# Kernel optimization log

Measured on AMD Instinct MI355X. Metric: run time of the kernel, lower is better.

## Reference

```python
import jax, jax.numpy as jnp
import numpy as np

N_NODES = 100000
N_EDGES = 3200000
N_GRAPHS = 512
IN_CH = 128
HID = 32
OUT = 2


def setup_inputs() -> dict:
    key = jax.random.key(0)
    ks = jax.random.split(key, 6)
    x = jax.random.normal(ks[0], (N_NODES, IN_CH), dtype=jnp.float32)
    edge_index = jax.random.randint(ks[1], (2, N_EDGES), 0, N_NODES, dtype=jnp.int64)
    batch = jnp.sort(jax.random.randint(ks[2], (N_NODES,), 0, N_GRAPHS, dtype=jnp.int64))
    # Glorot-ish params
    W1 = jax.random.normal(ks[3], (IN_CH, HID), dtype=jnp.float32) * (1.0 / np.sqrt(IN_CH))
    b1 = jnp.zeros((HID,), dtype=jnp.float32)
    W2 = jax.random.normal(ks[4], (HID, HID), dtype=jnp.float32) * (1.0 / np.sqrt(HID))
    b2 = jnp.zeros((HID,), dtype=jnp.float32)
    Wl = jax.random.normal(ks[5], (HID, OUT), dtype=jnp.float32) * (1.0 / np.sqrt(HID))
    bl = jnp.zeros((OUT,), dtype=jnp.float32)
    return {"x": x, "edge_index": edge_index, "batch": batch,
            "W1": W1, "b1": b1, "W2": W2, "b2": b2, "Wl": Wl, "bl": bl}


def _gcn_conv(h, src, dst, W, b, n_nodes):
    # PyG GCNConv: transform, add self-loops, symmetric deg normalization,
    # scatter-add messages from src -> dst, then bias.
    h = h @ W  # [N, F_out]
    ones = jnp.ones(src.shape[0], dtype=h.dtype)
    # degree on target nodes, +1 for the implicit self-loop
    deg = jax.ops.segment_sum(ones, dst, num_segments=n_nodes) + 1.0
    dinv = jax.lax.rsqrt(deg)  # deg >= 1 always
    norm = dinv[src] * dinv[dst]  # [E]
    agg = jax.ops.segment_sum(h[src] * norm[:, None], dst, num_segments=n_nodes)
    # self-loop contribution: norm_ii = dinv_i^2
    agg = agg + h * (dinv * dinv)[:, None]
    return agg + b


def reference(x, edge_index, batch, W1, b1, W2, b2, Wl, bl):
    n_nodes = x.shape[0]
    src, dst = edge_index[0], edge_index[1]
    h = jax.nn.relu(_gcn_conv(x, src, dst, W1, b1, n_nodes))
    h = jax.nn.relu(_gcn_conv(h, src, dst, W2, b2, n_nodes))
    # global mean pool per graph
    sums = jax.ops.segment_sum(h, batch, num_segments=N_GRAPHS)
    counts = jax.ops.segment_sum(jnp.ones(n_nodes, h.dtype), batch, num_segments=N_GRAPHS)
    pooled = sums / jnp.maximum(counts, 1.0)[:, None]  # [G, 32]
    return pooled @ Wl + bl  # [G, 2]
```

## Files before the change

kernel.cpp:

```cpp
#include <hip/hip_runtime.h>
#include <hip/hip_bf16.h>

#define N_NODES 100000
#define N_EDGES 3200000
#define N_GRAPHS 512
#define NBUK 782
#define CAP 4608
#define FILL_CHUNK 8192
#define FILL_BLOCKS ((N_EDGES + FILL_CHUNK - 1) / FILL_CHUNK)
#define GEMM1_BLOCKS ((N_NODES + 63) / 64)

__device__ __forceinline__ float blo(unsigned v) { return __uint_as_float(v << 16); }
__device__ __forceinline__ float bhi(unsigned v) { return __uint_as_float(v & 0xffff0000u); }

__global__ __launch_bounds__(1024) void k_fatA(const int* __restrict__ ei,
                                               int* __restrict__ gcnt,
                                               unsigned* __restrict__ packed,
                                               const float* __restrict__ x,
                                               const float* __restrict__ W1,
                                               float* __restrict__ H1u) {
    __shared__ __align__(16) char smem[49152];
    int t = threadIdx.x;
    if (blockIdx.x < FILL_BLOCKS) {
        unsigned* buf = (unsigned*)smem;
        int* h    = (int*)(smem + 32768);
        int* base = (int*)(smem + 35896);
        int* sb   = (int*)(smem + 39024);
        int* sc   = (int*)(smem + 42152);
        for (int i = t; i < NBUK; i += 1024) h[i] = 0;
        __syncthreads();
        int s0 = blockIdx.x * FILL_CHUNK;
        int ng = min(FILL_CHUNK, N_EDGES - s0) >> 2;
        const int4* src4 = (const int4*)(ei + s0);
        const int4* dst4 = (const int4*)(ei + N_EDGES + s0);
        int4 sv[2], dv[2];
        int  rk[2][4];
#pragma unroll
        for (int g = 0; g < 2; g++) {
            int gi = t + g * 1024;
            if (gi < ng) {
                sv[g] = src4[gi];
                dv[g] = dst4[gi];
                rk[g][0] = atomicAdd(&h[dv[g].x >> 7], 1);
                rk[g][1] = atomicAdd(&h[dv[g].y >> 7], 1);
                rk[g][2] = atomicAdd(&h[dv[g].z >> 7], 1);
                rk[g][3] = atomicAdd(&h[dv[g].w >> 7], 1);
            }
        }
        __syncthreads();
        for (int i = t; i < NBUK; i += 1024) {
            int c = h[i];
            base[i] = c ? atomicAdd(&gcnt[i], c) : 0;
        }
        sc[t] = (t < NBUK) ? h[t] : 0;
        __syncthreads();
        for (int off = 1; off < 1024; off <<= 1) {
            int v = (t >= off) ? sc[t - off] : 0;
            __syncthreads();
            sc[t] += v;
            __syncthreads();
        }
        for (int i = t; i < NBUK; i += 1024) sb[i] = sc[i] - h[i];
        __syncthreads();
#pragma unroll
        for (int g = 0; g < 2; g++) {
            int gi = t + g * 1024;
            if (gi < ng) {
                int s[4] = {sv[g].x, sv[g].y, sv[g].z, sv[g].w};
                int d[4] = {dv[g].x, dv[g].y, dv[g].z, dv[g].w};
#pragma unroll
                for (int k = 0; k < 4; k++) {
                    int bk = d[k] >> 7;
                    buf[sb[bk] + rk[g][k]] = (unsigned)s[k] | (((unsigned)d[k] & 127u) << 17);
                }
            }
        }
        __syncthreads();
        int w = t >> 6, lane = t & 63;
        for (int bk = w; bk < NBUK; bk += 16) {
            int c = h[bk];
            if (!c) continue;
            unsigned* gp = packed + (size_t)bk * CAP + base[bk];
            int lb = sb[bk];
            for (int j = lane; j < c; j += 64) gp[j] = buf[lb + j];
        }
    } else {
        float* Ws = (float*)smem;
        float* xs = (float*)(smem + 16384);
        int b = blockIdx.x - FILL_BLOCKS;
        ((float4*)Ws)[t] = ((const float4*)W1)[t];
        int row0 = b * 64;
        const float4* x4 = (const float4*)(x + (size_t)row0 * 128);
        float4* xs4 = (float4*)xs;
        int maxr = min(64, N_NODES - row0);
        int nf4 = maxr * 32;
#pragma unroll
        for (int i = 0; i < 8; i++) {
            int idx = t + i * 1024;
            if (idx < nf4) xs4[idx] = x4[idx];
        }
        __syncthreads();
        int col = t & 31;
        int g = t >> 5;
        int r0 = 2 * g, r1 = 2 * g + 1;
        const float4* xa4 = xs4 + r0 * 32;
        const float4* xb4 = xs4 + r1 * 32;
        float a0 = 0.f, a1 = 0.f;
#pragma unroll 8
        for (int k4 = 0; k4 < 32; k4++) {
            float4 xa = xa4[k4];
            float4 xb = xb4[k4];
            float w0 = Ws[(k4 * 4 + 0) * 32 + col];
            float w1 = Ws[(k4 * 4 + 1) * 32 + col];
            float w2 = Ws[(k4 * 4 + 2) * 32 + col];
            float w3 = Ws[(k4 * 4 + 3) * 32 + col];
            a0 += xa.x * w0 + xa.y * w1 + xa.z * w2 + xa.w * w3;
            a1 += xb.x * w0 + xb.y * w1 + xb.z * w2 + xb.w * w3;
        }
        if (row0 + r0 < N_NODES) H1u[(size_t)(row0 + r0) * 32 + col] = a0;
        if (row0 + r1 < N_NODES) H1u[(size_t)(row0 + r1) * 32 + col] = a1;
    }
}

__global__ __launch_bounds__(512) void k_csr(const unsigned* __restrict__ packed,
                                             const int* __restrict__ gcnt,
                                             int* __restrict__ rp, int* __restrict__ rpe,
                                             float* __restrict__ dinv,
                                             int* __restrict__ csr,
                                             const float* __restrict__ H1u,
                                             __hip_bfloat16* __restrict__ H1s) {
    __shared__ int deg[128];
    __shared__ int sd[128];
    __shared__ int nb0[128];
    __shared__ float dsh[128];
    __shared__ int lcsr[CAP] __attribute__((aligned(16)));
    int t = threadIdx.x;
    int b = blockIdx.x;
    if (t < 128) deg[t] = 0;
    __syncthreads();
    int n = gcnt[b];
    const unsigned* pb = packed + (size_t)b * CAP;
    unsigned pv[3][4];
    int rk[3][4];
#pragma unroll
    for (int g = 0; g < 3; g++) {
        int i0 = 4 * (t + g * 512);
        if (i0 < n) {
            if (i0 + 3 < n) {
                uint4 p = *(const uint4*)(pb + i0);
                pv[g][0] = p.x; pv[g][1] = p.y; pv[g][2] = p.z; pv[g][3] = p.w;
            } else {
#pragma unroll
                for (int k = 0; k < 4; k++) pv[g][k] = (i0 + k < n) ? pb[i0 + k] : 0u;
            }
#pragma unroll
            for (int k = 0; k < 4; k++)
                if (i0 + k < n) rk[g][k] = atomicAdd(&deg[pv[g][k] >> 17], 1);
        }
    }
    __syncthreads();
    int d = (t < 128) ? deg[t] : 0;
    if (t < 128) sd[t] = d;
    __syncthreads();
    for (int off = 1; off < 128; off <<= 1) {
        int v = (t >= off && t < 128) ? sd[t - off] : 0;
        __syncthreads();
        if (t < 128) sd[t] += v;
        __syncthreads();
    }
    if (t < 128) {
        int l0 = sd[t] - d;
        nb0[t] = l0;
        float di = rsqrtf((float)d + 1.0f);
        dsh[t] = di;
        int node = b * 128 + t;
        if (node < N_NODES) {
            rp[node] = b * CAP + l0;
            rpe[node] = b * CAP + l0 + d;
            dinv[node] = di;
        }
    }
    __syncthreads();
#pragma unroll
    for (int g = 0; g < 3; g++) {
        int i0 = 4 * (t + g * 512);
        if (i0 < n) {
#pragma unroll
            for (int k = 0; k < 4; k++) {
                if (i0 + k < n) {
                    unsigned p = pv[g][k];
                    lcsr[nb0[p >> 17] + rk[g][k]] = (int)(p & 0x1FFFFu);
                }
            }
        }
    }
    __syncthreads();
    int n4 = (n + 3) >> 2;
    int4* dst4 = (int4*)(csr + (size_t)b * CAP);
    const int4* sl4 = (const int4*)lcsr;
    for (int i = t; i < n4; i += 512) dst4[i] = sl4[i];
    for (int i = t; i < 1024; i += 512) {
        int row = i >> 3, q = i & 7;
        int node = b * 128 + row;
        if (node < N_NODES) {
            float4 v = ((const float4*)H1u)[(size_t)node * 8 + q];
            float di = dsh[row];
            __hip_bfloat16 tmp[4];
            tmp[0] = __float2bfloat16(v.x * di);
            tmp[1] = __float2bfloat16(v.y * di);
            tmp[2] = __float2bfloat16(v.z * di);
            tmp[3] = __float2bfloat16(v.w * di);
            *(uint2*)(H1s + (size_t)node * 32 + q * 4) = *(uint2*)tmp;
        }
    }
}

__global__ void k_gather(const __hip_bfloat16* __restrict__ Hs, const float* __restrict__ dinv,
                         const int* __restrict__ rp, const int* __restrict__ rpe,
                         const int* __restrict__ csr,
                         const float* __restrict__ bias, float* __restrict__ hout) {
    int wid = (blockIdx.x * 256 + threadIdx.x) >> 6;
    if (wid >= N_NODES) return;
    const uint4* H4 = (const uint4*)Hs;
    int lane = threadIdx.x & 63;
    int fb = lane & 3;
    int es = lane >> 2;
    int beg = rp[wid];
    int deg = rpe[wid] - beg;
    float a0=0.f,a1=0.f,a2=0.f,a3=0.f,a4=0.f,a5=0.f,a6=0.f,a7=0.f;
    for (int eb = 0; eb < deg; eb += 64) {
        int cv = csr[beg + eb + lane];
#pragma unroll
        for (int k = 0; k < 4; k++) {
            int e = eb + es + 16 * k;
            int src = __shfl(cv, es + 16 * k);
            if (e < deg) {
                uint4 v = H4[(size_t)src * 4 + fb];
                a0 += blo(v.x); a1 += bhi(v.x);
                a2 += blo(v.y); a3 += bhi(v.y);
                a4 += blo(v.z); a5 += bhi(v.z);
                a6 += blo(v.w); a7 += bhi(v.w);
            }
        }
    }
#pragma unroll
    for (int m = 4; m <= 32; m <<= 1) {
        a0 += __shfl_xor(a0, m); a1 += __shfl_xor(a1, m);
        a2 += __shfl_xor(a2, m); a3 += __shfl_xor(a3, m);
        a4 += __shfl_xor(a4, m); a5 += __shfl_xor(a5, m);
        a6 += __shfl_xor(a6, m); a7 += __shfl_xor(a7, m);
    }
    if (es == 0) {
        float di = dinv[wid];
        uint4 vw = H4[(size_t)wid * 4 + fb];
        float4 bA = *(const float4*)(bias + fb * 8);
        float4 bB = *(const float4*)(bias + fb * 8 + 4);
        float4 oA, oB;
        oA.x = fmaxf((a0 + blo(vw.x)) * di + bA.x, 0.f);
        oA.y = fmaxf((a1 + bhi(vw.x)) * di + bA.y, 0.f);
        oA.z = fmaxf((a2 + blo(vw.y)) * di + bA.z, 0.f);
        oA.w = fmaxf((a3 + bhi(vw.y)) * di + bA.w, 0.f);
        oB.x = fmaxf((a4 + blo(vw.z)) * di + bB.x, 0.f);
        oB.y = fmaxf((a5 + bhi(vw.z)) * di + bB.y, 0.f);
        oB.z = fmaxf((a6 + blo(vw.w)) * di + bB.z, 0.f);
        oB.w = fmaxf((a7 + bhi(vw.w)) * di + bB.w, 0.f);
        float* o = hout + (size_t)wid * 32 + fb * 8;
        *(float4*)o = oA;
        *(float4*)(o + 4) = oB;
    }
}

__global__ void k_gemm2(const float* __restrict__ h1, const float* __restrict__ W2,
                        const float* __restrict__ dinv, __hip_bfloat16* __restrict__ H2s) {
    __shared__ float Ws[32 * 32];
    __shared__ float xs[32 * 32];
    int t = threadIdx.x;
    ((float4*)Ws)[t] = ((const float4*)W2)[t];
    int row0 = blockIdx.x * 32;
    ((float4*)xs)[t] = ((const float4*)(h1 + (size_t)row0 * 32))[t];
    __syncthreads();
    int col = t & 31;
    int rb = (t >> 5) * 4;
    float a0 = 0.f, a1 = 0.f, a2 = 0.f, a3 = 0.f;
#pragma unroll
    for (int k = 0; k < 32; k++) {
        float w = Ws[k * 32 + col];
        a0 += xs[(rb + 0) * 32 + k] * w;
        a1 += xs[(rb + 1) * 32 + k] * w;
        a2 += xs[(rb + 2) * 32 + k] * w;
        a3 += xs[(rb + 3) * 32 + k] * w;
    }
    int r = row0 + rb;
    __hip_bfloat16* o = H2s + (size_t)r * 32 + col;
    o[0]  = __float2bfloat16(a0 * dinv[r + 0]);
    o[32] = __float2bfloat16(a1 * dinv[r + 1]);
    o[64] = __float2bfloat16(a2 * dinv[r + 2]);
    o[96] = __float2bfloat16(a3 * dinv[r + 3]);
}

__global__ __launch_bounds__(256) void k_pool(const float* __restrict__ h2,
                                              const int* __restrict__ batch,
                                              const float* __restrict__ Wl,
                                              const float* __restrict__ bl,
                                              float* __restrict__ out) {
    __shared__ float red[256];
    __shared__ float pooled[32];
    int g = blockIdx.x;
    int t = threadIdx.x;
    int lo = 0, hi = N_NODES;
    while (lo < hi) { int m = (lo + hi) >> 1; if (batch[m] < g) lo = m + 1; else hi = m; }
    int s = lo;
    hi = N_NODES;
    while (lo < hi) { int m = (lo + hi) >> 1; if (batch[m] < g + 1) lo = m + 1; else hi = m; }
    int e = lo;
    int f = t & 31, r0 = t >> 5;
    float acc = 0.f;
    for (int r = s + r0; r < e; r += 8) acc += h2[(size_t)r * 32 + f];
    red[t] = acc;
    __syncthreads();
    for (int off = 128; off >= 32; off >>= 1) {
        if (t < off) red[t] += red[t + off];
        __syncthreads();
    }
    if (t < 32) pooled[t] = red[t] / fmaxf((float)(e - s), 1.0f);
    __syncthreads();
    if (t < 2) {
        float a = bl[t];
#pragma unroll
        for (int k = 0; k < 32; k++) a += pooled[k] * Wl[k * 2 + t];
        out[g * 2 + t] = a;
    }
}

extern "C" void kernel_launch(void* const* d_in, const int* in_sizes, int n_in,
                              void* d_out, int out_size, void* d_ws, size_t ws_size,
                              hipStream_t stream) {
    const float* x    = (const float*)d_in[0];
    const int*   ei   = (const int*)d_in[1];
    const int*   batch= (const int*)d_in[2];
    const float* W1   = (const float*)d_in[3];
    const float* b1   = (const float*)d_in[4];
    const float* W2   = (const float*)d_in[5];
    const float* b2   = (const float*)d_in[6];
    const float* Wl   = (const float*)d_in[7];
    const float* bl   = (const float*)d_in[8];
    float* out = (float*)d_out;

    char* w = (char*)d_ws;
    size_t off = 0;
    auto take = [&](size_t bytes) -> char* {
        char* p = w + off;
        off = (off + bytes + 255) & ~(size_t)255;
        return p;
    };
    __hip_bfloat16* H1s = (__hip_bfloat16*)take((size_t)N_NODES * 32 * 2);
    float*          h1  = (float*)take((size_t)N_NODES * 32 * 4);
    char*           shared = take((size_t)NBUK * CAP * 4);
    unsigned*       packed = (unsigned*)shared;
    __hip_bfloat16* H2s    = (__hip_bfloat16*)shared;
    int*      csr    = (int*)  take((size_t)NBUK * CAP * 4 + 1024);
    float*    dinv   = (float*)take((size_t)N_NODES * 4);
    int*      rp     = (int*)  take((size_t)N_NODES * 4);
    int*      rpe    = (int*)  take((size_t)N_NODES * 4);
    int*      gcnt   = (int*)  take((size_t)NBUK * 4);

    hipMemsetAsync(gcnt, 0, (size_t)NBUK * 4, stream);

    k_fatA  <<<FILL_BLOCKS + GEMM1_BLOCKS, 1024, 0, stream>>>(ei, gcnt, packed, x, W1, h1);
    k_csr   <<<NBUK, 512, 0, stream>>>(packed, gcnt, rp, rpe, dinv, csr, h1, H1s);
    k_gather<<<N_NODES / 4, 256, 0, stream>>>(H1s, dinv, rp, rpe, csr, b1, h1);
    k_gemm2 <<<N_NODES / 32, 256, 0, stream>>>(h1, W2, dinv, H2s);
    k_gather<<<N_NODES / 4, 256, 0, stream>>>(H2s, dinv, rp, rpe, csr, b2, h1);
    k_pool  <<<N_GRAPHS, 256, 0, stream>>>(h1, batch, Wl, bl, out);
}
```

Baseline: 282.4 us.

## Pad CSR rows to multiples of 16 with dummy zero node; wave-shuffle scans

Each node's CSR adjacency list is padded to a multiple of 16 entries, filled with a sentinel index that points at an extra all-zero feature row appended to H1s and H2s. This lets the gather kernel drop the per-edge bounds check, using one uniform check per group of 16. The shared-memory Hillis-Steele prefix scans in the fill and CSR kernels are replaced with wavefront shuffle scans to cut barriers. In exchange the CSR grows, and the padding adds extra gathers of the zero row.

```diff
diff --git a/kernel.cpp b/kernel.cpp
--- a/kernel.cpp
+++ b/kernel.cpp
@@ -6,6 +6,7 @@
 #define N_GRAPHS 512
 #define NBUK 782
 #define CAP 4608
+#define CCAP 5632
 #define FILL_CHUNK 8192
 #define FILL_BLOCKS ((N_EDGES + FILL_CHUNK - 1) / FILL_CHUNK)
 #define GEMM1_BLOCKS ((N_NODES + 63) / 64)
@@ -26,7 +27,7 @@
         int* h    = (int*)(smem + 32768);
         int* base = (int*)(smem + 35896);
         int* sb   = (int*)(smem + 39024);
-        int* sc   = (int*)(smem + 42152);
+        int* ws   = (int*)(smem + 42152);
         for (int i = t; i < NBUK; i += 1024) h[i] = 0;
         __syncthreads();
         int s0 = blockIdx.x * FILL_CHUNK;
@@ -52,15 +53,28 @@
             int c = h[i];
             base[i] = c ? atomicAdd(&gcnt[i], c) : 0;
         }
-        sc[t] = (t < NBUK) ? h[t] : 0;
-        __syncthreads();
-        for (int off = 1; off < 1024; off <<= 1) {
-            int v = (t >= off) ? sc[t - off] : 0;
-            __syncthreads();
-            sc[t] += v;
-            __syncthreads();
-        }
-        for (int i = t; i < NBUK; i += 1024) sb[i] = sc[i] - h[i];
+        int lane = t & 63, wv = t >> 6;
+        int hval = (t < NBUK) ? h[t] : 0;
+        int v = hval;
+#pragma unroll
+        for (int d2 = 1; d2 < 64; d2 <<= 1) {
+            int o = __shfl_up(v, d2);
+            if (lane >= d2) v += o;
+        }
+        if (lane == 63) ws[wv] = v;
+        __syncthreads();
+        if (wv == 0) {
+            int s = (lane < 16) ? ws[lane] : 0;
+            int sv2 = s;
+#pragma unroll
+            for (int d2 = 1; d2 < 16; d2 <<= 1) {
+                int o = __shfl_up(sv2, d2);
+                if (lane >= d2) sv2 += o;
+            }
+            if (lane < 16) ws[lane] = sv2 - s;
+        }
+        __syncthreads();
+        if (t < NBUK) sb[t] = v + ws[wv] - hval;
         __syncthreads();
 #pragma unroll
         for (int g = 0; g < 2; g++) {
@@ -76,7 +90,7 @@
             }
         }
         __syncthreads();
-        int w = t >> 6, lane = t & 63;
+        int w = t >> 6;
         for (int bk = w; bk < NBUK; bk += 16) {
             int c = h[bk];
             if (!c) continue;
@@ -130,10 +144,11 @@
                                              const float* __restrict__ H1u,
                                              __hip_bfloat16* __restrict__ H1s) {
     __shared__ int deg[128];
-    __shared__ int sd[128];
     __shared__ int nb0[128];
     __shared__ float dsh[128];
-    __shared__ int lcsr[CAP] __attribute__((aligned(16)));
+    __shared__ int wsum0;
+    __shared__ int ntot;
+    __shared__ int lcsr[CCAP] __attribute__((aligned(16)));
     int t = threadIdx.x;
     int b = blockIdx.x;
     if (t < 128) deg[t] = 0;
@@ -159,26 +174,31 @@
         }
     }
     __syncthreads();
+    int lane = t & 63;
     int d = (t < 128) ? deg[t] : 0;
-    if (t < 128) sd[t] = d;
-    __syncthreads();
-    for (int off = 1; off < 128; off <<= 1) {
-        int v = (t >= off && t < 128) ? sd[t - off] : 0;
-        __syncthreads();
-        if (t < 128) sd[t] += v;
-        __syncthreads();
-    }
+    int p16 = (d + 15) & ~15;
+    int v = (t < 128) ? p16 : 0;
+#pragma unroll
+    for (int d2 = 1; d2 < 64; d2 <<= 1) {
+        int o = __shfl_up(v, d2);
+        if (lane >= d2) v += o;
+    }
+    if (t == 63) wsum0 = v;
+    __syncthreads();
     if (t < 128) {
-        int l0 = sd[t] - d;
+        int inc = v + ((t >= 64) ? wsum0 : 0);
+        int l0 = inc - p16;
         nb0[t] = l0;
         float di = rsqrtf((float)d + 1.0f);
         dsh[t] = di;
         int node = b * 128 + t;
         if (node < N_NODES) {
-            rp[node] = b * CAP + l0;
-            rpe[node] = b * CAP + l0 + d;
+            rp[node] = b * CCAP + l0;
+            rpe[node] = b * CCAP + l0 + p16;
             dinv[node] = di;
         }
+        for (int j = d; j < p16; j++) lcsr[l0 + j] = N_NODES;
+        if (t == 127) ntot = l0 + p16;
     }
     __syncthreads();
 #pragma unroll
@@ -195,24 +215,25 @@
         }
     }
     __syncthreads();
-    int n4 = (n + 3) >> 2;
-    int4* dst4 = (int4*)(csr + (size_t)b * CAP);
+    int nq = (ntot + 3) >> 2;
+    int4* dst4 = (int4*)(csr + (size_t)b * CCAP);
     const int4* sl4 = (const int4*)lcsr;
-    for (int i = t; i < n4; i += 512) dst4[i] = sl4[i];
+    for (int i = t; i < nq; i += 512) dst4[i] = sl4[i];
     for (int i = t; i < 1024; i += 512) {
         int row = i >> 3, q = i & 7;
         int node = b * 128 + row;
         if (node < N_NODES) {
-            float4 v = ((const float4*)H1u)[(size_t)node * 8 + q];
+            float4 fv = ((const float4*)H1u)[(size_t)node * 8 + q];
             float di = dsh[row];
             __hip_bfloat16 tmp[4];
-            tmp[0] = __float2bfloat16(v.x * di);
-            tmp[1] = __float2bfloat16(v.y * di);
-            tmp[2] = __float2bfloat16(v.z * di);
-            tmp[3] = __float2bfloat16(v.w * di);
+            tmp[0] = __float2bfloat16(fv.x * di);
+            tmp[1] = __float2bfloat16(fv.y * di);
+            tmp[2] = __float2bfloat16(fv.z * di);
+            tmp[3] = __float2bfloat16(fv.w * di);
             *(uint2*)(H1s + (size_t)node * 32 + q * 4) = *(uint2*)tmp;
         }
     }
+    if (b == 0 && t < 16) ((unsigned*)(H1s + (size_t)N_NODES * 32))[t] = 0u;
 }
 
 __global__ void k_gather(const __hip_bfloat16* __restrict__ Hs, const float* __restrict__ dinv,
@@ -226,15 +247,14 @@
     int fb = lane & 3;
     int es = lane >> 2;
     int beg = rp[wid];
-    int deg = rpe[wid] - beg;
+    int pdeg = rpe[wid] - beg;
     float a0=0.f,a1=0.f,a2=0.f,a3=0.f,a4=0.f,a5=0.f,a6=0.f,a7=0.f;
-    for (int eb = 0; eb < deg; eb += 64) {
+    for (int eb = 0; eb < pdeg; eb += 64) {
         int cv = csr[beg + eb + lane];
 #pragma unroll
         for (int k = 0; k < 4; k++) {
-            int e = eb + es + 16 * k;
-            int src = __shfl(cv, es + 16 * k);
-            if (e < deg) {
+            if (eb + 16 * k < pdeg) {
+                int src = __shfl(cv, es + 16 * k);
                 uint4 v = H4[(size_t)src * 4 + fb];
                 a0 += blo(v.x); a1 += bhi(v.x);
                 a2 += blo(v.y); a3 += bhi(v.y);
@@ -296,6 +316,7 @@
     o[32] = __float2bfloat16(a1 * dinv[r + 1]);
     o[64] = __float2bfloat16(a2 * dinv[r + 2]);
     o[96] = __float2bfloat16(a3 * dinv[r + 3]);
+    if (blockIdx.x == 0 && t < 16) ((unsigned*)(H2s + (size_t)N_NODES * 32))[t] = 0u;
 }
 
 __global__ __launch_bounds__(256) void k_pool(const float* __restrict__ h2,
@@ -353,12 +374,12 @@
         off = (off + bytes + 255) & ~(size_t)255;
         return p;
     };
-    __hip_bfloat16* H1s = (__hip_bfloat16*)take((size_t)N_NODES * 32 * 2);
+    __hip_bfloat16* H1s = (__hip_bfloat16*)take((size_t)(N_NODES + 1) * 32 * 2);
     float*          h1  = (float*)take((size_t)N_NODES * 32 * 4);
     char*           shared = take((size_t)NBUK * CAP * 4);
     unsigned*       packed = (unsigned*)shared;
     __hip_bfloat16* H2s    = (__hip_bfloat16*)shared;
-    int*      csr    = (int*)  take((size_t)NBUK * CAP * 4 + 1024);
+    int*      csr    = (int*)  take((size_t)NBUK * CCAP * 4 + 1024);
     float*    dinv   = (float*)take((size_t)N_NODES * 4);
     int*      rp     = (int*)  take((size_t)N_NODES * 4);
     int*      rpe    = (int*)  take((size_t)N_NODES * 4);
```

Result: no change. 282.7 us (+0.1%).
